# Kernel tuning notes

Hardware: AMD Instinct MI355X
Metric: run time of the kernel (lower is better)

The kernel has to match this reference:

```python
import jax, jax.numpy as jnp
import numpy as np

N = 50000
E = 800000
D = 128
H = 8
HD = D // H


def setup_inputs() -> dict:
    key = jax.random.key(0)
    ks = jax.random.split(key, 12)
    s = 1.0 / np.sqrt(D)
    x = jax.random.normal(ks[0], (N, D), dtype=jnp.float32)
    edge_index = jax.random.randint(ks[1], (2, E), 0, N, dtype=jnp.int64)
    edge_bias = jax.random.normal(ks[2], (E, H), dtype=jnp.float32)
    Wq = jax.random.uniform(ks[3], (D, D), jnp.float32, -s, s)
    bq = jax.random.uniform(ks[4], (D,), jnp.float32, -s, s)
    Wk = jax.random.uniform(ks[5], (D, D), jnp.float32, -s, s)
    bk = jax.random.uniform(ks[6], (D,), jnp.float32, -s, s)
    Wv = jax.random.uniform(ks[7], (D, D), jnp.float32, -s, s)
    bv = jax.random.uniform(ks[8], (D,), jnp.float32, -s, s)
    Wo = jax.random.uniform(ks[9], (D, D), jnp.float32, -s, s)
    bo = jax.random.uniform(ks[10], (D,), jnp.float32, -s, s)
    return {"x": x, "edge_index": edge_index, "edge_bias": edge_bias,
            "Wq": Wq, "bq": bq, "Wk": Wk, "bk": bk,
            "Wv": Wv, "bv": bv, "Wo": Wo, "bo": bo}


def reference(x, edge_index, edge_bias, Wq, bq, Wk, bk, Wv, bv, Wo, bo):
    scale = HD ** -0.5
    row, col = edge_index[0], edge_index[1]
    # Node-level projections -> [N, H, HD]
    q = (x @ Wq + bq).reshape(N, H, HD)
    k = (x @ Wk + bk).reshape(N, H, HD)
    v = (x @ Wv + bv).reshape(N, H, HD)
    # Edge-level gather + per-edge attention logits [E, H]
    q_i = q[col]
    k_j = k[row]
    v_j = v[row]
    attn = jnp.einsum('ehd,ehd->eh', q_i, k_j) * scale + edge_bias
    # Scatter-softmax over incoming edges of each destination node (col)
    seg_max = jax.ops.segment_max(attn, col, num_segments=N)  # [N, H]
    seg_max = jnp.where(jnp.isfinite(seg_max), seg_max, 0.0)  # empty segments -> 0
    ex = jnp.exp(attn - seg_max[col])
    denom = jax.ops.segment_sum(ex, col, num_segments=N)      # [N, H]
    attn = ex / (denom[col] + 1e-16)
    # Scatter-add weighted values -> [N, H, HD]
    weighted_v = attn[:, :, None] * v_j
    out = jax.ops.segment_sum(weighted_v, col, num_segments=N)
    out = out.reshape(N, D)
    return out @ Wo + bo
```

## Files before the change

kernel.cpp:

```cpp
#include <hip/hip_runtime.h>
#include <math.h>

#define NN 50000
#define EE 800000
#define DD 128
#define HH 8
#define HDD 16
#define CAP 64
#define NSTRIP 3125
#define QB 782
#define PREB 3907
#define LTS 130

typedef __attribute__((ext_vector_type(8))) short short8;
typedef __attribute__((ext_vector_type(4))) float f32x4;

union U8 { ushort u[8]; int4 v; short8 s; };

__device__ __forceinline__ ushort f2bf(float f) {
    uint u = __float_as_uint(f);
    uint r = (u + 0x7fffu + ((u >> 16) & 1u)) >> 16;
    return (ushort)r;
}
__device__ __forceinline__ float bf2f(ushort u) {
    return __uint_as_float(((uint)u) << 16);
}

__global__ void k_prep(const float* __restrict__ Wq, const float* __restrict__ Wk,
                       const float* __restrict__ Wv, const float* __restrict__ Wo,
                       const float* __restrict__ bq, const float* __restrict__ bk,
                       const float* __restrict__ bv, const float* __restrict__ bo,
                       ushort* __restrict__ Wt, float* __restrict__ bpack) {
    int tid = blockIdx.x * 256 + threadIdx.x;
    int w = tid >> 14, rem = tid & 16383, c = rem >> 7, i = rem & 127;
    const float* W = (w == 0) ? Wq : (w == 1) ? Wk : (w == 2) ? Wv : Wo;
    float s = (w == 0) ? 0.25f : 1.0f;
    Wt[(size_t)w * 16384 + c * 128 + i] = f2bf(W[i * 128 + c] * s);
    if (i == 0) {
        const float* B = (w == 0) ? bq : (w == 1) ? bk : (w == 2) ? bv : bo;
        bpack[w * 128 + c] = B[c] * s;
    }
}

__global__ __launch_bounds__(256) void k_pre(
    const float* __restrict__ x, const ushort* __restrict__ Wt,
    const float* __restrict__ bpk,
    ushort* __restrict__ qb, ushort* __restrict__ kk, ushort* __restrict__ vv,
    const int* __restrict__ col, const int* __restrict__ row,
    int* __restrict__ cursor, int2* __restrict__ reB) {
    __shared__ ushort T[4][16 * LTS];
    int tid = threadIdx.x;
    int b = blockIdx.x;

    if (b % 5 != 0) {
        int fi = b - b / 5 - 1;
        int e = fi * 256 + tid;
        if (e < EE) {
            int c = col[e];
            int p = atomicAdd(&cursor[c], 1);
            if (p < CAP) reB[(size_t)c * CAP + p] = make_int2(row[e], e);
        }
        return;
    }

    int wave = tid >> 6, lane = tid & 63;
    int strip = (b / 5) * 4 + wave;
    if (strip >= NSTRIP) return;
    int r0 = strip * 16;
    int lr = lane & 15, lg = lane >> 4;
    ushort* Tw = T[wave];

    short8 afr[4];
    const float* xp = x + (size_t)(r0 + lr) * 128;
#pragma unroll
    for (int ks = 0; ks < 4; ks++) {
        const float* ap = xp + ks * 32 + lg * 8;
        float4 f0 = *(const float4*)ap;
        float4 f1 = *(const float4*)(ap + 4);
        U8 r;
        r.u[0] = f2bf(f0.x); r.u[1] = f2bf(f0.y); r.u[2] = f2bf(f0.z); r.u[3] = f2bf(f0.w);
        r.u[4] = f2bf(f1.x); r.u[5] = f2bf(f1.y); r.u[6] = f2bf(f1.z); r.u[7] = f2bf(f1.w);
        afr[ks] = r.s;
    }

    for (int w = 0; w < 3; w++) {
        f32x4 acc[8];
#pragma unroll
        for (int n = 0; n < 8; n++) acc[n] = (f32x4){0.f, 0.f, 0.f, 0.f};
        const ushort* Wb = Wt + (size_t)w * 16384;
#pragma unroll
        for (int ks = 0; ks < 4; ks++) {
            short8 bfr[8];
#pragma unroll
            for (int n = 0; n < 8; n++)
                bfr[n] = *(const short8*)&Wb[(n * 16 + lr) * 128 + ks * 32 + lg * 8];
#pragma unroll
            for (int n = 0; n < 8; n++)
                acc[n] = __builtin_amdgcn_mfma_f32_16x16x32_bf16(afr[ks], bfr[n], acc[n], 0, 0, 0);
        }

#pragma unroll
        for (int n = 0; n < 8; n++) {
            float bv_ = bpk[w * 128 + n * 16 + lr];
#pragma unroll
            for (int rg = 0; rg < 4; rg++)
                Tw[(lg * 4 + rg) * LTS + n * 16 + lr] = f2bf(acc[n][rg] + bv_);
        }
        ushort* dst = (w == 0) ? qb : (w == 1) ? kk : vv;
#pragma unroll
        for (int i = 0; i < 4; i++) {
            int4 vd = *(const int4*)&Tw[(i * 4 + lg) * LTS + lr * 8];
            *(int4*)&dst[(size_t)(r0 + i * 4 + lg) * 128 + lr * 8] = vd;
        }
    }
}

__global__ __launch_bounds__(256) void k_gemm_out(
    const ushort* __restrict__ A, const ushort* __restrict__ Bt,
    const float* __restrict__ bias, float* __restrict__ Cf) {
    int tid = threadIdx.x;
    int wave = tid >> 6, lane = tid & 63;
    int strip = blockIdx.x * 4 + wave;
    if (strip >= NSTRIP) return;
    int r0 = strip * 16;
    int lr = lane & 15, lg = lane >> 4;

    short8 afr[4];
#pragma unroll
    for (int ks = 0; ks < 4; ks++)
        afr[ks] = *(const short8*)&A[(size_t)(r0 + lr) * 128 + ks * 32 + lg * 8];

    f32x4 acc[8];
#pragma unroll
    for (int n = 0; n < 8; n++) acc[n] = (f32x4){0.f, 0.f, 0.f, 0.f};
#pragma unroll
    for (int ks = 0; ks < 4; ks++) {
        short8 bfr[8];
#pragma unroll
        for (int n = 0; n < 8; n++)
            bfr[n] = *(const short8*)&Bt[(n * 16 + lr) * 128 + ks * 32 + lg * 8];
#pragma unroll
        for (int n = 0; n < 8; n++)
            acc[n] = __builtin_amdgcn_mfma_f32_16x16x32_bf16(afr[ks], bfr[n], acc[n], 0, 0, 0);
    }
#pragma unroll
    for (int n = 0; n < 8; n++) {
        int gcol = n * 16 + lr;
        float bv_ = bias[gcol];
#pragma unroll
        for (int rg = 0; rg < 4; rg++) {
            int grow = r0 + lg * 4 + rg;
            Cf[(size_t)grow * 128 + gcol] = acc[n][rg] + bv_;
        }
    }
}

__global__ __launch_bounds__(256) void k_attn(
    const ushort* __restrict__ qb, const ushort* __restrict__ kk,
    const ushort* __restrict__ vv, const float* __restrict__ ebias,
    const int2* __restrict__ reB, const int* __restrict__ deg,
    ushort* __restrict__ aggb) {
    int wave = threadIdx.x >> 6;
    int lane = threadIdx.x & 63;
    int n = blockIdx.x * 4 + wave;
    if (n >= NN) return;
    int cnt = min(deg[n], CAP);
    const int2* bucket = reB + (size_t)n * CAP;
    int h = lane >> 3;
    int j = lane & 7;
    int hb = lane & ~7;

    float qf[16];
    {
        U8 q0, q1;
        const ushort* qp = qb + (size_t)n * DD + h * HDD;
        q0.v = *(const int4*)qp;
        q1.v = *(const int4*)(qp + 8);
#pragma unroll
        for (int t = 0; t < 8; t++) qf[t] = bf2f(q0.u[t]);
#pragma unroll
        for (int t = 0; t < 8; t++) qf[8 + t] = bf2f(q1.u[t]);
    }

    float m = -INFINITY;
    float denom = 0.f;
    float acc0 = 0.f, acc1 = 0.f;

    for (int idx = 0; idx < cnt; idx += 8) {
        int my = idx + j;
        bool valid = my < cnt;
        int2 re = valid ? bucket[my] : make_int2(0, 0);
        int r = re.x;
        float logit = -INFINITY;
        if (valid) {
            const ushort* kp = kk + (size_t)r * DD + h * HDD;
            U8 a0, a1;
            a0.v = *(const int4*)kp;
            a1.v = *(const int4*)(kp + 8);
            float d = 0.f;
#pragma unroll
            for (int t = 0; t < 8; t++) d += qf[t] * bf2f(a0.u[t]);
#pragma unroll
            for (int t = 0; t < 8; t++) d += qf[8 + t] * bf2f(a1.u[t]);
            logit = d + ebias[(size_t)re.y * HH + h];
        }
        float cm = logit;
        cm = fmaxf(cm, __shfl_xor(cm, 1));
        cm = fmaxf(cm, __shfl_xor(cm, 2));
        cm = fmaxf(cm, __shfl_xor(cm, 4));
        float mnew = fmaxf(m, cm);
        float sc = __expf(m - mnew);
        float p = __expf(logit - mnew);
        m = mnew;
        float ps = p;
        ps += __shfl_xor(ps, 1);
        ps += __shfl_xor(ps, 2);
        ps += __shfl_xor(ps, 4);
        denom = denom * sc + ps;
        acc0 *= sc;
        acc1 *= sc;
#pragma unroll
        for (int j2 = 0; j2 < 8; j2++) {
            float pj = __shfl(p, hb + j2);
            int rj = __shfl(r, hb + j2);
            uint vp = *(const uint*)(vv + (size_t)rj * DD + 2 * lane);
            acc0 += pj * bf2f((ushort)(vp & 0xffffu));
            acc1 += pj * bf2f((ushort)(vp >> 16));
        }
    }
    float inv = 1.0f / (denom + 1e-16f);
    uint pack = (uint)f2bf(acc0 * inv) | ((uint)f2bf(acc1 * inv) << 16);
    *(uint*)&aggb[(size_t)n * DD + 2 * lane] = pack;
}

extern "C" void kernel_launch(void* const* d_in, const int* in_sizes, int n_in,
                              void* d_out, int out_size, void* d_ws, size_t ws_size,
                              hipStream_t stream) {
    const float* x     = (const float*)d_in[0];
    const int*   eidx  = (const int*)d_in[1];
    const float* ebias = (const float*)d_in[2];
    const float* Wq    = (const float*)d_in[3];
    const float* bq    = (const float*)d_in[4];
    const float* Wk    = (const float*)d_in[5];
    const float* bk    = (const float*)d_in[6];
    const float* Wv    = (const float*)d_in[7];
    const float* bv    = (const float*)d_in[8];
    const float* Wo    = (const float*)d_in[9];
    const float* bo    = (const float*)d_in[10];
    float* out = (float*)d_out;

    const int* row = eidx;
    const int* col = eidx + EE;

    char* p = (char*)d_ws;
    ushort* qb    = (ushort*)p;  p += (size_t)NN * DD * 2;
    ushort* kk    = (ushort*)p;  p += (size_t)NN * DD * 2;
    ushort* vvp   = (ushort*)p;  p += (size_t)NN * DD * 2;
    ushort* aggb  = (ushort*)p;  p += (size_t)NN * DD * 2;
    ushort* Wt    = (ushort*)p;  p += (size_t)4 * 16384 * 2;
    float*  bpk   = (float*)p;   p += 4 * 128 * 4;
    int2*   reB   = (int2*)p;    p += (size_t)NN * CAP * 8;
    int* cursor   = (int*)p;     p += (size_t)NN * 4;

    hipMemsetAsync(cursor, 0, (size_t)NN * sizeof(int), stream);

    hipLaunchKernelGGL(k_prep, dim3(256), dim3(256), 0, stream,
                       Wq, Wk, Wv, Wo, bq, bk, bv, bo, Wt, bpk);

    hipLaunchKernelGGL(k_pre, dim3(PREB), dim3(256), 0, stream,
                       x, Wt, bpk, qb, kk, vvp, col, row, cursor, reB);

    hipLaunchKernelGGL(k_attn, dim3(NN / 4), dim3(256), 0, stream,
                       qb, kk, vvp, ebias, reB, cursor, aggb);

    hipLaunchKernelGGL(k_gemm_out, dim3(QB), dim3(256), 0, stream,
                       aggb, Wt + 3 * 16384, bpk + 3 * 128, out);
}
```

Baseline: 181.8 us.

## Partition CSR bucket fill by XCD so node-range atomics stay XCD-local

```diff
diff --git a/kernel.cpp b/kernel.cpp
--- a/kernel.cpp
+++ b/kernel.cpp
@@ -7,9 +7,13 @@
 #define HH 8
 #define HDD 16
 #define CAP 64
+#define NXCD 8
+#define NPG 6250
+#define SL 2048
+#define NSL 391
 #define NSTRIP 3125
 #define QB 782
-#define PREB 3907
+#define FILLB 3128
 #define LTS 130
 
 typedef __attribute__((ext_vector_type(8))) short short8;
@@ -52,19 +56,34 @@
     int tid = threadIdx.x;
     int b = blockIdx.x;
 
-    if (b % 5 != 0) {
-        int fi = b - b / 5 - 1;
-        int e = fi * 256 + tid;
-        if (e < EE) {
-            int c = col[e];
-            int p = atomicAdd(&cursor[c], 1);
-            if (p < CAP) reB[(size_t)c * CAP + p] = make_int2(row[e], e);
+    if (b >= QB) {
+        int fi = b - QB;
+        int g = b & 7;
+        int j = fi >> 3;
+        int lo = g * NPG, hi = lo + NPG;
+        int base = j * SL + tid * 8;
+        if (base < EE) {
+            int4 c0 = *(const int4*)&col[base];
+            int4 c1 = *(const int4*)&col[base + 4];
+            int cs[8] = {c0.x, c0.y, c0.z, c0.w, c1.x, c1.y, c1.z, c1.w};
+            int lim = EE - base;
+#pragma unroll
+            for (int t = 0; t < 8; t++) {
+                if (t < lim) {
+                    int c = cs[t];
+                    if (c >= lo && c < hi) {
+                        int e = base + t;
+                        int p = atomicAdd(&cursor[c], 1);
+                        if (p < CAP) reB[(size_t)c * CAP + p] = make_int2(row[e], e);
+                    }
+                }
+            }
         }
         return;
     }
 
     int wave = tid >> 6, lane = tid & 63;
-    int strip = (b / 5) * 4 + wave;
+    int strip = b * 4 + wave;
     if (strip >= NSTRIP) return;
     int r0 = strip * 16;
     int lr = lane & 15, lg = lane >> 4;
@@ -267,12 +286,12 @@
     hipLaunchKernelGGL(k_prep, dim3(256), dim3(256), 0, stream,
                        Wq, Wk, Wv, Wo, bq, bk, bv, bo, Wt, bpk);
 
-    hipLaunchKernelGGL(k_pre, dim3(PREB), dim3(256), 0, stream,
+    hipLaunchKernelGGL(k_pre, dim3(QB + FILLB), dim3(256), 0, stream,
                        x, Wt, bpk, qb, kk, vvp, col, row, cursor, reB);
 
     hipLaunchKernelGGL(k_attn, dim3(NN / 4), dim3(256), 0, stream,
                        qb, kk, vvp, ebias, reB, cursor, aggb);
 
-    hipLaunchKernelGGL(k_gemm_out, dim3(QB), dim3(256), 0, stream,
+    hipLaunchKernelGGL(k_gemm_out, dim3((NSTRIP + 3) / 4), dim3(256), 0, stream,
                        aggb, Wt + 3 * 16384, bpk + 3 * 128, out);
 }
```

After: 178.1 us. 1.02x faster.
